# Optimization experiments

Measured on AMD Instinct MI355X. Metric: run time of the kernel, lower is better.

## Reference

```python
import jax, jax.numpy as jnp
import numpy as np

RADIUS = 5.0
CORRECT_THRESHOLD = 0.5
NUM_CLASSES = 4
COORD_RANGE = 64.0  # keep coords in a small field so some preds actually match


def setup_inputs() -> dict:
    key = jax.random.key(0)
    k1, k2, k3, k4 = jax.random.split(key, 4)
    B, P, T = 16, 4096, 1024
    pred_cls = jax.random.randint(k1, (B, P, 1), 0, NUM_CLASSES).astype(jnp.float32)
    pred_xy = jax.random.uniform(k2, (B, P, 2), dtype=jnp.float32) * COORD_RANGE
    gt_cls = jax.random.randint(k3, (B, T, 1), 0, NUM_CLASSES).astype(jnp.float32)
    gt_xy = jax.random.uniform(k4, (B, T, 2), dtype=jnp.float32) * COORD_RANGE
    pred = jnp.concatenate([pred_cls, pred_xy], axis=-1)  # [B,P,3]
    gt = jnp.concatenate([gt_cls, gt_xy], axis=-1)        # [B,T,3]
    return {"pred": pred, "gt": gt}


def _radial_score(centers, targets):
    # centers: [B,P,2], targets: [B,T,2] -> [B,P,T]; sigmoid(1 - dist/radius)
    d = centers[:, :, None, :] - targets[:, None, :, :]
    dist = jnp.sqrt(jnp.sum(d * d, axis=-1))
    return jax.nn.sigmoid(1.0 - dist / RADIUS)


def reference(pred, gt):
    B, P, _ = pred.shape
    T = gt.shape[1]
    classes = pred[:, :, 0]          # [B,P]
    centers = pred[:, :, 1:3]        # [B,P,2]
    tclasses = gt[:, :, 0]           # [B,T]
    tcenters = gt[:, :, 1:3]         # [B,T,2]

    scores = _radial_score(centers, tcenters)                       # [B,P,T]
    valid = (scores >= CORRECT_THRESHOLD) & (
        classes[:, :, None] == tclasses[:, None, :])                # [B,P,T]

    # Greedy dedup (sort-by-score + unique on target col) keeps, per target,
    # its highest-scoring valid pred; the second unique (pred col) only drops
    # duplicate preds and never changes the set of matched pred indices.
    masked = jnp.where(valid, scores, -jnp.inf)
    best_pred = jnp.argmax(masked, axis=1)                          # [B,T]
    has_match = jnp.any(valid, axis=1)                              # [B,T]

    flat_idx = (best_pred + jnp.arange(B, dtype=best_pred.dtype)[:, None] * P).ravel()
    hits = jnp.zeros((B * P,), jnp.float32).at[flat_idx].add(
        has_match.ravel().astype(jnp.float32))
    correct = hits.reshape(B, P) > 0                                # [B,P]

    tp = correct.sum().astype(jnp.float32)
    fp = jnp.float32(B * P) - tp
    fn = jnp.float32(B * T) - tp

    eps = jnp.float32(1e-6)
    precision = (tp + eps) / (tp + eps + fp + eps)
    recall = (tp + eps) / (tp + fn + eps)
    f1 = 2.0 * precision * recall / (precision + recall)
    return 1.0 - f1
```

## Files before the change

kernel.cpp:

```cpp
#include <hip/hip_runtime.h>
#include <math.h>

#define BB 16
#define PP 4096
#define TT 1024
#define JT 8
#define HALF 2048
#define LIMKEY 0x41C80FFFu

__global__ __launch_bounds__(256) void match_kernel(const float* __restrict__ pred,
                                                    const float* __restrict__ gt,
                                                    unsigned* __restrict__ part) {
    const int blk   = blockIdx.x;
    const int b     = blk >> 6;
    const int ttile = (blk >> 1) & 31;
    const int half  = blk & 1;
    const int wave  = threadIdx.x >> 6;
    const int lane  = threadIdx.x & 63;
    const int tbase = ttile * 32 + wave * JT;
    const int pbase = half * HALF;

    const float* gb = gt + ((size_t)(b * TT + tbase)) * 3;
    float gx[JT], gy[JT];
    unsigned key[JT];
    #pragma unroll
    for (int j = 0; j < JT; ++j) {
        const float c = gb[j * 3 + 0];
        gx[j] = fmaf(c, 128.0f, gb[j * 3 + 1]);
        gy[j] = gb[j * 3 + 2];
        key[j] = 0xFFFFFFFFu;
    }

    const float* pl = pred + (size_t)b * PP * 3 + (size_t)(pbase + lane) * 3;

    #pragma unroll 4
    for (int i = 0; i < HALF / 64; ++i) {
        const float pc = pl[0];
        const float px = pl[1];
        const float py = pl[2];
        pl += 192;
        const float pxp = fmaf(pc, 128.0f, px);
        const unsigned po = (unsigned)(pbase + (i << 6) + lane);
        #pragma unroll
        for (int j = 0; j < JT; ++j) {
            const float dx = pxp - gx[j];
            const float dy = py - gy[j];
            const float d2 = fmaf(dx, dx, dy * dy);
            const unsigned kk = (__float_as_uint(d2) & 0xFFFFF000u) | po;
            key[j] = min(key[j], kk);
        }
    }

    for (int off = 32; off; off >>= 1) {
        #pragma unroll
        for (int j = 0; j < JT; ++j) {
            const unsigned o = __shfl_down(key[j], off, 64);
            key[j] = min(key[j], o);
        }
    }

    if (lane == 0) {
        #pragma unroll
        for (int j = 0; j < JT; ++j)
            part[(size_t)half * (BB * TT) + b * TT + tbase + j] = key[j];
    }
}

__global__ __launch_bounds__(1024) void count_kernel(const unsigned* __restrict__ part,
                                                     float* __restrict__ out) {
    __shared__ unsigned bm[BB * PP / 32];
    for (int i = threadIdx.x; i < BB * PP / 32; i += 1024) bm[i] = 0;
    __syncthreads();

    for (int i = threadIdx.x; i < BB * TT; i += 1024) {
        const unsigned k = min(part[i], part[BB * TT + i]);
        if (k <= LIMKEY) {
            const unsigned g = (unsigned)(i >> 10) * PP + (k & 0xFFFu);
            atomicOr(&bm[g >> 5], 1u << (g & 31));
        }
    }
    __syncthreads();

    int sum = 0;
    for (int i = threadIdx.x; i < BB * PP / 32; i += 1024) sum += __popc(bm[i]);
    for (int off = 32; off; off >>= 1) sum += __shfl_down(sum, off, 64);

    __shared__ int ss[16];
    const int wid  = threadIdx.x >> 6;
    const int lane = threadIdx.x & 63;
    if (lane == 0) ss[wid] = sum;
    __syncthreads();
    if (threadIdx.x == 0) {
        int tp_i = 0;
        for (int w = 0; w < 16; ++w) tp_i += ss[w];
        const float tp = (float)tp_i;
        const float eps = 1e-6f;
        const float fp = (float)(BB * PP) - tp;
        const float fn = (float)(BB * TT) - tp;
        const float precision = (tp + eps) / (tp + eps + fp + eps);
        const float recall    = (tp + eps) / (tp + fn + eps);
        const float f1 = 2.0f * precision * recall / (precision + recall);
        out[0] = 1.0f - f1;
    }
}

extern "C" void kernel_launch(void* const* d_in, const int* in_sizes, int n_in,
                              void* d_out, int out_size, void* d_ws, size_t ws_size,
                              hipStream_t stream) {
    const float* pred = (const float*)d_in[0];
    const float* gt   = (const float*)d_in[1];
    float* out = (float*)d_out;
    unsigned* part = (unsigned*)d_ws;

    match_kernel<<<BB * TT / 32 * 2, 256, 0, stream>>>(pred, gt, part);
    count_kernel<<<1, 1024, 0, stream>>>(part, out);
}
```

Baseline: 73.50 us.

## Split pred range into quarters, widen target tile, parallelize count per batch

The match kernel now gives each wave 16 targets instead of 8 and splits the prediction range into four quarters instead of two. This doubles register reuse of each loaded prediction while keeping the block count unchanged. The single-block count kernel is replaced by 16 per-batch blocks, each with its own small shared bitmap, followed by a tiny kernel that computes F1. This removes a serialized single-block tail but adds one extra kernel launch and a fourth partial buffer to read.

```diff
diff --git a/kernel.cpp b/kernel.cpp
--- a/kernel.cpp
+++ b/kernel.cpp
@@ -4,8 +4,8 @@
 #define BB 16
 #define PP 4096
 #define TT 1024
-#define JT 8
-#define HALF 2048
+#define JT 16
+#define QTR 1024
 #define LIMKEY 0x41C80FFFu
 
 __global__ __launch_bounds__(256) void match_kernel(const float* __restrict__ pred,
@@ -13,12 +13,12 @@
                                                     unsigned* __restrict__ part) {
     const int blk   = blockIdx.x;
     const int b     = blk >> 6;
-    const int ttile = (blk >> 1) & 31;
-    const int half  = blk & 1;
+    const int ttile = (blk >> 2) & 15;
+    const int qtr   = blk & 3;
     const int wave  = threadIdx.x >> 6;
     const int lane  = threadIdx.x & 63;
-    const int tbase = ttile * 32 + wave * JT;
-    const int pbase = half * HALF;
+    const int tbase = ttile * 64 + wave * JT;
+    const int pbase = qtr * QTR;
 
     const float* gb = gt + ((size_t)(b * TT + tbase)) * 3;
     float gx[JT], gy[JT];
@@ -34,7 +34,7 @@
     const float* pl = pred + (size_t)b * PP * 3 + (size_t)(pbase + lane) * 3;
 
     #pragma unroll 4
-    for (int i = 0; i < HALF / 64; ++i) {
+    for (int i = 0; i < QTR / 64; ++i) {
         const float pc = pl[0];
         const float px = pl[1];
         const float py = pl[2];
@@ -62,38 +62,41 @@
     if (lane == 0) {
         #pragma unroll
         for (int j = 0; j < JT; ++j)
-            part[(size_t)half * (BB * TT) + b * TT + tbase + j] = key[j];
+            part[(size_t)qtr * (BB * TT) + b * TT + tbase + j] = key[j];
     }
 }
 
-__global__ __launch_bounds__(1024) void count_kernel(const unsigned* __restrict__ part,
-                                                     float* __restrict__ out) {
-    __shared__ unsigned bm[BB * PP / 32];
-    for (int i = threadIdx.x; i < BB * PP / 32; i += 1024) bm[i] = 0;
+__global__ __launch_bounds__(256) void count_kernel(const unsigned* __restrict__ part,
+                                                    int* __restrict__ psum) {
+    __shared__ unsigned bm[PP / 32];
+    if (threadIdx.x < 128) bm[threadIdx.x] = 0;
     __syncthreads();
 
-    for (int i = threadIdx.x; i < BB * TT; i += 1024) {
-        const unsigned k = min(part[i], part[BB * TT + i]);
+    const int b = blockIdx.x;
+    const unsigned* pb = part + b * TT;
+    for (int i = threadIdx.x; i < TT; i += 256) {
+        unsigned k = min(min(pb[i], pb[BB * TT + i]),
+                         min(pb[2 * BB * TT + i], pb[3 * BB * TT + i]));
         if (k <= LIMKEY) {
-            const unsigned g = (unsigned)(i >> 10) * PP + (k & 0xFFFu);
-            atomicOr(&bm[g >> 5], 1u << (g & 31));
+            const unsigned p = k & 0xFFFu;
+            atomicOr(&bm[p >> 5], 1u << (p & 31));
         }
     }
     __syncthreads();
 
-    int sum = 0;
-    for (int i = threadIdx.x; i < BB * PP / 32; i += 1024) sum += __popc(bm[i]);
+    int sum = (threadIdx.x < 128) ? (int)__popc(bm[threadIdx.x]) : 0;
     for (int off = 32; off; off >>= 1) sum += __shfl_down(sum, off, 64);
+    __shared__ int ss[4];
+    if ((threadIdx.x & 63) == 0) ss[threadIdx.x >> 6] = sum;
+    __syncthreads();
+    if (threadIdx.x == 0) psum[b] = ss[0] + ss[1] + ss[2] + ss[3];
+}
 
-    __shared__ int ss[16];
-    const int wid  = threadIdx.x >> 6;
-    const int lane = threadIdx.x & 63;
-    if (lane == 0) ss[wid] = sum;
-    __syncthreads();
+__global__ void f1_kernel(const int* __restrict__ psum, float* __restrict__ out) {
+    int v = (threadIdx.x < BB) ? psum[threadIdx.x] : 0;
+    for (int off = 32; off; off >>= 1) v += __shfl_down(v, off, 64);
     if (threadIdx.x == 0) {
-        int tp_i = 0;
-        for (int w = 0; w < 16; ++w) tp_i += ss[w];
-        const float tp = (float)tp_i;
+        const float tp = (float)v;
         const float eps = 1e-6f;
         const float fp = (float)(BB * PP) - tp;
         const float fn = (float)(BB * TT) - tp;
@@ -110,8 +113,11 @@
     const float* pred = (const float*)d_in[0];
     const float* gt   = (const float*)d_in[1];
     float* out = (float*)d_out;
+
     unsigned* part = (unsigned*)d_ws;
+    int* psum = (int*)((char*)d_ws + 4 * BB * TT * 4);
 
-    match_kernel<<<BB * TT / 32 * 2, 256, 0, stream>>>(pred, gt, part);
-    count_kernel<<<1, 1024, 0, stream>>>(part, out);
+    match_kernel<<<BB * 16 * 4, 256, 0, stream>>>(pred, gt, part);
+    count_kernel<<<BB, 256, 0, stream>>>(part, psum);
+    f1_kernel<<<1, 64, 0, stream>>>(psum, out);
 }
```

After: 70.75 us, median of 2. 3.7% less time.
